# Kernel tuning notes

Hardware: AMD Instinct MI355X
Metric: run time of the kernel (lower is better)

## Reference

```python
import jax, jax.numpy as jnp
import numpy as np

N, F_IN, HID, HEADS, NEA, E, G = 50000, 32, 64, 2, 2, 800000, 50
SLOPE = 0.2  # leaky_relu negative_slope


def setup_inputs() -> dict:
    key = jax.random.key(0)
    ks = jax.random.split(key, 24)
    x = jax.random.normal(ks[0], (N, F_IN), jnp.float32)
    src = jax.random.randint(ks[1], (E,), 0, N, jnp.int32)
    off = jax.random.randint(ks[2], (E,), 1, N, jnp.int32)
    dst = ((src + off) % N).astype(jnp.int32)  # guaranteed no self loops
    edge_index = jnp.stack([src, dst])
    edge_attr = jax.random.uniform(ks[3], (E, NEA), jnp.float32, 0.5, 3.0)  # distances (reciprocal taken in fwd)
    batch = (jnp.arange(N) // (N // G)).astype(jnp.int32)
    interface_pos = jnp.arange(0, N, 5, dtype=jnp.int32)  # 200 interface nodes/graph

    def glorot(k, shape, fan_in, fan_out):
        s = jnp.sqrt(6.0 / (fan_in + fan_out))
        return jax.random.uniform(k, shape, jnp.float32, -s, s)

    HC = HEADS * HID
    W0 = glorot(ks[4], (F_IN, HC), F_IN, HC)
    attl0 = glorot(ks[5], (HEADS, HID), HID, HID)
    attr0 = glorot(ks[6], (HEADS, HID), HID, HID)
    W12 = glorot(ks[7], (2, HID, HC), HID, HC)
    attl12 = glorot(ks[8], (2, HEADS, HID), HID, HID)
    attr12 = glorot(ks[9], (2, HEADS, HID), HID, HID)
    eW = glorot(ks[10], (3, NEA, HC), NEA, HC)
    eb = jnp.zeros((3, HC), jnp.float32)
    bconv = jnp.zeros((3, HID), jnp.float32)
    gate_w = glorot(ks[11], (HID, 1), HID, 1)
    gate_b = jnp.zeros((1,), jnp.float32)
    lin1_w = glorot(ks[12], (4 * HID, 2 * HID), 4 * HID, 2 * HID)
    lin1_b = jnp.zeros((2 * HID,), jnp.float32)
    lin2_w = glorot(ks[13], (2 * HID, 1), 2 * HID, 1)
    lin2_b = jnp.zeros((1,), jnp.float32)
    return dict(x=x, edge_index=edge_index, edge_attr=edge_attr, batch=batch,
                interface_pos=interface_pos, graph_num=G,
                W0=W0, attl0=attl0, attr0=attr0, W12=W12, attl12=attl12, attr12=attr12,
                eW=eW, eb=eb, bconv=bconv, gate_w=gate_w, gate_b=gate_b,
                lin1_w=lin1_w, lin1_b=lin1_b, lin2_w=lin2_w, lin2_b=lin2_b)


def segment_softmax(e, seg, n):
    m = jax.ops.segment_max(e, seg, num_segments=n)
    ex = jnp.exp(e - m[seg])
    d = jax.ops.segment_sum(ex, seg, num_segments=n)
    return ex / (d[seg] + 1e-16)


def gate_conv(h, W, att_l, att_r, eW, eb, b, src, dst, ea):
    # GATEConv, concat=False, dropout in eval mode (identity)
    n = h.shape[0]
    H, C = att_l.shape
    xl = (h @ W).reshape(n, H, C)                      # lin_l == lin_r
    al = (xl * att_l).sum(-1)                          # [N,H]
    ar = (xl * att_r).sum(-1)
    e = jax.nn.leaky_relu(al[src] + ar[dst], SLOPE)    # [E+N,H]
    alpha = segment_softmax(e, dst, n)
    ee = (ea @ eW + eb).reshape(-1, H, C)              # edge embeddings
    msg = (xl[src] + ee) * alpha[..., None]
    out = jax.ops.segment_sum(msg, dst, num_segments=n)
    return out.mean(1) + b                             # mean over heads + bias


def reference(x, edge_index, edge_attr, batch, interface_pos, graph_num,
              W0, attl0, attr0, W12, attl12, attr12, eW, eb, bconv,
              gate_w, gate_b, lin1_w, lin1_b, lin2_w, lin2_b):
    n = x.shape[0]
    ar_n = jnp.arange(n, dtype=edge_index.dtype)
    src = jnp.concatenate([edge_index[0], ar_n])       # add self loops
    dst = jnp.concatenate([edge_index[1], ar_n])
    ea = jnp.concatenate([1.0 / edge_attr,
                          jnp.zeros((n, edge_attr.shape[1]), edge_attr.dtype)], 0)

    h = jnp.tanh(gate_conv(x, W0, attl0, attr0, eW[0], eb[0], bconv[0], src, dst, ea))
    xmax = h
    for l in range(2):  # num_layers - 1 structurally distinct weight slices
        h = jnp.tanh(gate_conv(h, W12[l], attl12[l], attr12[l],
                               eW[l + 1], eb[l + 1], bconv[l + 1], src, dst, ea))
        xmax = jnp.maximum(xmax, h)                    # JumpingKnowledge('max')

    xi = xmax[interface_pos]                           # [Ni, hidden]
    bi = batch[interface_pos]
    add = jax.ops.segment_sum(xi, bi, num_segments=graph_num)
    cnt = jax.ops.segment_sum(jnp.ones((xi.shape[0],), xi.dtype), bi, num_segments=graph_num)
    mean = add / jnp.maximum(cnt, 1.0)[:, None]
    gate = (xi @ gate_w + gate_b)[:, 0]                # global self-attention gate
    a = segment_softmax(gate, bi, graph_num)
    attp = jax.ops.segment_sum(a[:, None] * xi, bi, num_segments=graph_num)
    mx = jax.ops.segment_max(xi, bi, num_segments=graph_num)
    pooled = jnp.concatenate([add, mean, attp, mx], -1)  # [G, 4*hidden]
    z = jnp.tanh(pooled @ lin1_w + lin1_b)             # dropout eval = identity
    return z @ lin2_w + lin2_b                         # [G, 1]
```

## Files before the change

### kernel.cpp

```cpp
#include <hip/hip_runtime.h>
#include <hip/hip_bf16.h>
#include <hip/hip_fp16.h>
#include <math.h>

#define N_NODES 50000
#define FIN     32
#define HID     64
#define HC      128
#define NE      800000
#define NET     850000
#define NI      10000
#define NG      50
#define NPG     1000
#define NIPG    200
#define DMAX    64

#define LBLK    (N_NODES / 16)
#define ABLK    (N_NODES / 8)

typedef _Float16 half8 __attribute__((ext_vector_type(8)));
typedef float float4v __attribute__((ext_vector_type(4)));

__device__ __forceinline__ float lrelu(float x) { return fmaxf(x, 0.2f * x); }

__device__ __forceinline__ float rlf(float v, int l) {
  return __int_as_float(__builtin_amdgcn_readlane(__float_as_int(v), l));
}
__device__ __forceinline__ int rli(int v, int l) {
  return __builtin_amdgcn_readlane(v, l);
}

__global__ void k_build(const int* __restrict__ ei, const float* __restrict__ eattr,
                        int* __restrict__ deg, int2* __restrict__ erec) {
  int e = blockIdx.x * blockDim.x + threadIdx.x;
  if (e >= NET) return;
  int s, d; float ex, ey;
  if (e < NE) {
    s = ei[e]; d = ei[NE + e];
    float2 ea = ((const float2*)eattr)[e];
    ex = 1.0f / ea.x; ey = 1.0f / ea.y;
  } else {
    s = d = e - NE; ex = 0.f; ey = 0.f;
  }
  int r = atomicAdd(&deg[d], 1);
  if (r < DMAX) {
    __half2 ea2 = __floats2half2_rn(ex, ey);
    erec[d * DMAX + r] = make_int2(s << 8, *(int*)&ea2);
  }
}

template <int F>
__global__ __launch_bounds__(256) void k_linear_mfma(
    const float* __restrict__ h, const float* __restrict__ W,
    const float* __restrict__ attl, const float* __restrict__ attr,
    __half2* __restrict__ xl2h, float* __restrict__ al, float* __restrict__ ar) {
  __shared__ _Float16 hA[16 * F];
  __shared__ _Float16 hC[16 * 128];
  __shared__ float redl[16 * 4], redr[16 * 4];
  const int w = threadIdx.x >> 6, lane = threadIdx.x & 63;
  const int m = lane & 15, q = lane >> 4;
  const int n0 = blockIdx.x * 16;

  for (int i = threadIdx.x; i < 16 * F; i += 256)
    hA[i] = (_Float16)h[(size_t)n0 * F + i];
  __syncthreads();

  half8 a0, a1;
#pragma unroll
  for (int j = 0; j < 8; j++) a0[j] = hA[m * F + q * 8 + j];
  if constexpr (F == 64) {
#pragma unroll
    for (int j = 0; j < 8; j++) a1[j] = hA[m * F + 32 + q * 8 + j];
  }

  const int c0 = w * 32;
  float4v acc[2];
  float pl[4] = {0.f, 0.f, 0.f, 0.f}, pr[4] = {0.f, 0.f, 0.f, 0.f};
#pragma unroll
  for (int t = 0; t < 2; t++) {
    const int colg = c0 + t * 16 + m;
    half8 b0;
#pragma unroll
    for (int j = 0; j < 8; j++) b0[j] = (_Float16)W[(q * 8 + j) * HC + colg];
    float4v z = {0.f, 0.f, 0.f, 0.f};
    acc[t] = __builtin_amdgcn_mfma_f32_16x16x32_f16(a0, b0, z, 0, 0, 0);
    if constexpr (F == 64) {
      half8 b1;
#pragma unroll
      for (int j = 0; j < 8; j++) b1[j] = (_Float16)W[(32 + q * 8 + j) * HC + colg];
      acc[t] = __builtin_amdgcn_mfma_f32_16x16x32_f16(a1, b1, acc[t], 0, 0, 0);
    }
    const float atl = attl[colg], atr = attr[colg];
#pragma unroll
    for (int reg = 0; reg < 4; reg++) {
      float val = acc[t][reg];
      hC[(q * 4 + reg) * 128 + colg] = (_Float16)val;
      pl[reg] += val * atl;
      pr[reg] += val * atr;
    }
  }
#pragma unroll
  for (int off = 1; off < 16; off <<= 1) {
#pragma unroll
    for (int reg = 0; reg < 4; reg++) {
      pl[reg] += __shfl_xor(pl[reg], off, 64);
      pr[reg] += __shfl_xor(pr[reg], off, 64);
    }
  }
  if (m == 0) {
#pragma unroll
    for (int reg = 0; reg < 4; reg++) {
      redl[(q * 4 + reg) * 4 + w] = pl[reg];
      redr[(q * 4 + reg) * 4 + w] = pr[reg];
    }
  }
  __syncthreads();
  if (threadIdx.x < 32) {
    int node = threadIdx.x >> 1, head = threadIdx.x & 1;
    al[(n0 + node) * 2 + head] = redl[node * 4 + head * 2] + redl[node * 4 + head * 2 + 1];
    ar[(n0 + node) * 2 + head] = redr[node * 4 + head * 2] + redr[node * 4 + head * 2 + 1];
  }
  for (int i = threadIdx.x; i < 16 * 64; i += 256) {
    int node = i >> 6, cc = i & 63;
    xl2h[(size_t)(n0 + node) * HID + cc] =
        __halves2half2(hC[node * 128 + cc], hC[node * 128 + 64 + cc]);
  }
}

__device__ __forceinline__ void agg_wave(
    int n0, const __half2* __restrict__ xl, const float* __restrict__ alp,
    const float2* __restrict__ ar2,
    const int* __restrict__ degarr, const int2* __restrict__ erec,
    const float* __restrict__ eW2, const float* __restrict__ eb1,
    const float* __restrict__ bconv1, float& outA, float& outB) {
  const int gid0 = n0 + ((threadIdx.x >> 6) << 1);
  const int lane = threadIdx.x & 63;
  const int l32 = lane & 31;
  const int half = lane >> 5;
  const int lane4 = lane << 2;
  const int gidH = gid0 + half;
  const int o0H = gidH * DMAX;
  const int degH = min(degarr[gidH], DMAX);
  const float2 arvH = ar2[gidH];
  const char* xbase = (const char*)xl;
  const char* albase = (const char*)alp;

  const int degA = rli(degH, 0);
  const int degB = rli(degH, 32);
  const int degmax = max(degA, degB);

  float aA0 = 0.f, aA1 = 0.f, bA0 = 0.f, bA1 = 0.f;
  float aB0 = 0.f, aB1 = 0.f, bB0 = 0.f, bB1 = 0.f;
  float ld0 = 0.f, ld1 = 0.f, lex0 = 0.f, ley0 = 0.f, lex1 = 0.f, ley1 = 0.f;

  for (int base = 0; base < degmax; base += 32) {
    int j = base + l32;
    int soff = 0; float p0 = 0.f, p1 = 0.f;
    if (j < degH) {
      int2 r = erec[o0H + j];
      soff = r.x;
      float2 eaf = __half22float2(*(__half2*)&r.y);
      float2 alv = *(const float2*)(albase + (soff >> 5));
      p0 = __expf(lrelu(alv.x + arvH.x));
      p1 = __expf(lrelu(alv.y + arvH.y));
      ld0 += p0; ld1 += p1;
      lex0 += p0 * eaf.x; ley0 += p0 * eaf.y;
      lex1 += p1 * eaf.x; ley1 += p1 * eaf.y;
    }
    int lenA = min(32, degA - base); lenA = max(lenA, 0);
    int lenB = min(32, degB - base); lenB = max(lenB, 0);
    int lenA4 = (lenA + 3) & ~3;
    int lenB4 = (lenB + 3) & ~3;
    int len = max(lenA4, lenB4);
    for (int j2 = 0; j2 < len; j2 += 4) {
      if (j2 < lenA4) {
        float2 x0 = __half22float2(*(const __half2*)(xbase + rli(soff, j2)     + lane4));
        float2 x1 = __half22float2(*(const __half2*)(xbase + rli(soff, j2 + 1) + lane4));
        float2 x2 = __half22float2(*(const __half2*)(xbase + rli(soff, j2 + 2) + lane4));
        float2 x3 = __half22float2(*(const __half2*)(xbase + rli(soff, j2 + 3) + lane4));
        aA0 += rlf(p0, j2)     * x0.x; aA1 += rlf(p1, j2)     * x0.y;
        bA0 += rlf(p0, j2 + 1) * x1.x; bA1 += rlf(p1, j2 + 1) * x1.y;
        aA0 += rlf(p0, j2 + 2) * x2.x; aA1 += rlf(p1, j2 + 2) * x2.y;
        bA0 += rlf(p0, j2 + 3) * x3.x; bA1 += rlf(p1, j2 + 3) * x3.y;
      }
      if (j2 < lenB4) {
        float2 x4 = __half22float2(*(const __half2*)(xbase + rli(soff, 32 + j2)     + lane4));
        float2 x5 = __half22float2(*(const __half2*)(xbase + rli(soff, 32 + j2 + 1) + lane4));
        float2 x6 = __half22float2(*(const __half2*)(xbase + rli(soff, 32 + j2 + 2) + lane4));
        float2 x7 = __half22float2(*(const __half2*)(xbase + rli(soff, 32 + j2 + 3) + lane4));
        aB0 += rlf(p0, 32 + j2)     * x4.x; aB1 += rlf(p1, 32 + j2)     * x4.y;
        bB0 += rlf(p0, 32 + j2 + 1) * x5.x; bB1 += rlf(p1, 32 + j2 + 1) * x5.y;
        aB0 += rlf(p0, 32 + j2 + 2) * x6.x; aB1 += rlf(p1, 32 + j2 + 2) * x6.y;
        bB0 += rlf(p0, 32 + j2 + 3) * x7.x; bB1 += rlf(p1, 32 + j2 + 3) * x7.y;
      }
    }
  }
  float accA0 = aA0 + bA0, accA1 = aA1 + bA1;
  float accB0 = aB0 + bB0, accB1 = aB1 + bB1;
#pragma unroll
  for (int off = 16; off; off >>= 1) {
    ld0  += __shfl_xor(ld0, off, 64);
    ld1  += __shfl_xor(ld1, off, 64);
    lex0 += __shfl_xor(lex0, off, 64);
    ley0 += __shfl_xor(ley0, off, 64);
    lex1 += __shfl_xor(lex1, off, 64);
    ley1 += __shfl_xor(ley1, off, 64);
  }
  float ld0A  = __shfl(ld0,  l32, 64), ld0B  = __shfl(ld0,  32 + l32, 64);
  float ld1A  = __shfl(ld1,  l32, 64), ld1B  = __shfl(ld1,  32 + l32, 64);
  float lex0A = __shfl(lex0, l32, 64), lex0B = __shfl(lex0, 32 + l32, 64);
  float ley0A = __shfl(ley0, l32, 64), ley0B = __shfl(ley0, 32 + l32, 64);
  float lex1A = __shfl(lex1, l32, 64), lex1B = __shfl(lex1, 32 + l32, 64);
  float ley1A = __shfl(ley1, l32, 64), ley1B = __shfl(ley1, 32 + l32, 64);

  const float w00 = eW2[lane],      w01 = eW2[HC + lane],      b0v = eb1[lane];
  const float w10 = eW2[64 + lane], w11 = eW2[HC + 64 + lane], b1v = eb1[64 + lane];
  const float bc = bconv1[lane];

  float tA0 = accA0 + w00 * lex0A + w01 * ley0A + b0v * ld0A;
  float tA1 = accA1 + w10 * lex1A + w11 * ley1A + b1v * ld1A;
  float tB0 = accB0 + w00 * lex0B + w01 * ley0B + b0v * ld0B;
  float tB1 = accB1 + w10 * lex1B + w11 * ley1B + b1v * ld1B;
  outA = tanhf(0.5f * (tA0 / (ld0A + 1e-16f) + tA1 / (ld1A + 1e-16f)) + bc);
  outB = tanhf(0.5f * (tB0 / (ld0B + 1e-16f) + tB1 / (ld1B + 1e-16f)) + bc);
}

__global__ __launch_bounds__(256) void k_aggregate(
    const __half2* __restrict__ xl_in, const float* __restrict__ al_in,
    const float2* __restrict__ ar2, const int* __restrict__ degarr,
    const int2* __restrict__ erec, const float* __restrict__ eW2,
    const float* __restrict__ eb1, const float* __restrict__ bconv1,
    float* __restrict__ hout) {
  const int n0 = blockIdx.x * 8;
  float rA, rB;
  agg_wave(n0, xl_in, al_in, ar2, degarr, erec, eW2, eb1, bconv1, rA, rB);
  const int gid0 = n0 + ((threadIdx.x >> 6) << 1);
  const int lane = threadIdx.x & 63;
  hout[(size_t)gid0 * HID + lane] = rA;
  hout[(size_t)(gid0 + 1) * HID + lane] = rB;
}

__global__ __launch_bounds__(256) void k_agg_xi(
    const __half2* __restrict__ xl_in, const float* __restrict__ al_in,
    const float2* __restrict__ ar2, const int* __restrict__ degarr,
    const int2* __restrict__ erec, const float* __restrict__ eW2,
    const float* __restrict__ eb1, const float* __restrict__ bconv1,
    const float* __restrict__ h0, const float* __restrict__ h1,
    const float* __restrict__ gate_w, const float* __restrict__ gate_b,
    float* __restrict__ xi, float* __restrict__ gexp) {
  const int n0 = blockIdx.x * 8;
  float rA, rB;
  agg_wave(n0, xl_in, al_in, ar2, degarr, erec, eW2, eb1, bconv1, rA, rB);
  const int gid0 = n0 + ((threadIdx.x >> 6) << 1);
  const int lane = threadIdx.x & 63;
  const int nA = gid0, nB = gid0 + 1;
  const float gwv = gate_w[lane];
  const float gbv = gate_b[0];
  if (nA % 5 == 0) {
    float v = fmaxf(fmaxf(h0[(size_t)nA * HID + lane], h1[(size_t)nA * HID + lane]), rA);
    int idx = nA / 5;
    xi[(size_t)idx * HID + lane] = v;
    float gv = v * gwv;
#pragma unroll
    for (int off = 32; off; off >>= 1) gv += __shfl_xor(gv, off, 64);
    if (lane == 0) gexp[idx] = __expf(gv + gbv);
  }
  if (nB % 5 == 0) {
    float v = fmaxf(fmaxf(h0[(size_t)nB * HID + lane], h1[(size_t)nB * HID + lane]), rB);
    int idx = nB / 5;
    xi[(size_t)idx * HID + lane] = v;
    float gv = v * gwv;
#pragma unroll
    for (int off = 32; off; off >>= 1) gv += __shfl_xor(gv, off, 64);
    if (lane == 0) gexp[idx] = __expf(gv + gbv);
  }
}

__global__ __launch_bounds__(256) void k_final(
    const float* __restrict__ xi, const float* __restrict__ gexp,
    const float* __restrict__ lin1_w, const float* __restrict__ lin1_b,
    const float* __restrict__ lin2_w, const float* __restrict__ lin2_b,
    float* __restrict__ out) {
  __shared__ float red[4][3 * HID + 1];
  __shared__ float pooled[4 * HID];
  __shared__ float zred[2 * HID];
  const int g = blockIdx.x, t = threadIdx.x;
  const int w = t >> 6, lane = t & 63;

  float padd = 0.f, pmax = -1e30f, pattp = 0.f, paden = 0.f;
  for (int i = w; i < NIPG; i += 4) {
    int idx = g * NIPG + i;
    float v = xi[(size_t)idx * HID + lane];
    float e = gexp[idx];
    padd += v;
    pmax = fmaxf(pmax, v);
    pattp += e * v;
    paden += e;
  }
  red[w][lane] = padd;
  red[w][HID + lane] = pmax;
  red[w][2 * HID + lane] = pattp;
  if (lane == 0) red[w][3 * HID] = paden;
  __syncthreads();
  if (t < HID) {
    float a  = red[0][t] + red[1][t] + red[2][t] + red[3][t];
    float mx = fmaxf(fmaxf(red[0][HID + t], red[1][HID + t]),
                     fmaxf(red[2][HID + t], red[3][HID + t]));
    float ap = red[0][2 * HID + t] + red[1][2 * HID + t] +
               red[2][2 * HID + t] + red[3][2 * HID + t];
    float ad = red[0][3 * HID] + red[1][3 * HID] + red[2][3 * HID] + red[3][3 * HID];
    pooled[t]           = a;
    pooled[HID + t]     = a * (1.0f / NIPG);
    pooled[2 * HID + t] = ap / (ad + 1e-16f);
    pooled[3 * HID + t] = mx;
  }
  __syncthreads();
  if (t < 2 * HID) {
    float z = lin1_b[t];
    for (int k = 0; k < 4 * HID; k++) z += pooled[k] * lin1_w[k * (2 * HID) + t];
    z = tanhf(z);
    zred[t] = z * lin2_w[t];
  }
  __syncthreads();
  if (t == 0) {
    float s = 0.f;
    for (int k = 0; k < 2 * HID; k++) s += zred[k];
    out[g] = s + lin2_b[0];
  }
}

extern "C" void kernel_launch(void* const* d_in, const int* in_sizes, int n_in,
                              void* d_out, int out_size, void* d_ws, size_t ws_size,
                              hipStream_t stream) {
  const float* x      = (const float*)d_in[0];
  const int*   ei     = (const int*)d_in[1];
  const float* eattr  = (const float*)d_in[2];
  const float* W0     = (const float*)d_in[6];
  const float* attl0  = (const float*)d_in[7];
  const float* attr0  = (const float*)d_in[8];
  const float* W12    = (const float*)d_in[9];
  const float* attl12 = (const float*)d_in[10];
  const float* attr12 = (const float*)d_in[11];
  const float* eW     = (const float*)d_in[12];
  const float* eb     = (const float*)d_in[13];
  const float* bconv  = (const float*)d_in[14];
  const float* gate_w = (const float*)d_in[15];
  const float* gate_b = (const float*)d_in[16];
  const float* lin1_w = (const float*)d_in[17];
  const float* lin1_b = (const float*)d_in[18];
  const float* lin2_w = (const float*)d_in[19];
  const float* lin2_b = (const float*)d_in[20];
  float* out = (float*)d_out;

  char* ws = (char*)d_ws;
  size_t off = 0;
  auto alloc = [&](size_t elems) {
    void* p = ws + off;
    off += ((elems * 4 + 15) / 16) * 16;
    return p;
  };
  int*      deg    = (int*)alloc(N_NODES);
  size_t zbytes = off;
  int2*    erec   = (int2*)alloc((size_t)N_NODES * DMAX * 2);
  __half2* xl2hA  = (__half2*)alloc((size_t)N_NODES * HID);
  __half2* xl2hB  = (__half2*)alloc((size_t)N_NODES * HID);
  float*   alA    = (float*)alloc((size_t)N_NODES * 2);
  float*   alB    = (float*)alloc((size_t)N_NODES * 2);
  float*   arr    = (float*)alloc((size_t)N_NODES * 2);
  float*   h0     = (float*)alloc((size_t)N_NODES * HID);
  float*   h1     = (float*)alloc((size_t)N_NODES * HID);
  float*   xi     = (float*)alloc((size_t)NI * HID);
  float*   gexp   = (float*)alloc(NI);
  (void)ws_size; (void)in_sizes; (void)n_in; (void)out_size;

  hipMemsetAsync(d_ws, 0, zbytes, stream);

  k_build<<<(NET + 255) / 256, 256, 0, stream>>>(ei, eattr, deg, erec);
  k_linear_mfma<FIN><<<LBLK, 256, 0, stream>>>(x, W0, attl0, attr0, xl2hA, alA, arr);
  k_aggregate<<<ABLK, 256, 0, stream>>>(xl2hA, alA, (const float2*)arr, deg, erec,
                                        eW, eb, bconv, h0);
  k_linear_mfma<HID><<<LBLK, 256, 0, stream>>>(h0, W12, attl12, attr12, xl2hB, alB, arr);
  k_aggregate<<<ABLK, 256, 0, stream>>>(xl2hB, alB, (const float2*)arr, deg, erec,
                                        eW + 2 * HC, eb + HC, bconv + HID, h1);
  k_linear_mfma<HID><<<LBLK, 256, 0, stream>>>(h1, W12 + (size_t)HID * HC,
                                               attl12 + HC, attr12 + HC, xl2hA, alA, arr);
  k_agg_xi<<<ABLK, 256, 0, stream>>>(xl2hA, alA, (const float2*)arr, deg, erec,
                                     eW + 4 * HC, eb + 2 * HC, bconv + 2 * HID,
                                     h0, h1, gate_w, gate_b, xi, gexp);
  k_final<<<NG, 256, 0, stream>>>(xi, gexp, lin1_w, lin1_b, lin2_w, lin2_b, out);
}
```

Baseline: 330.1 us.

## Fuse edge-build and first linear layer into one launch, vectorize edge loads

Merges the CSR-style edge bucketing kernel and the layer-0 MFMA linear kernel into a single launch: the first blocks process edges and the remaining blocks compute linear tiles, since the two are independent. The edge path now handles four edges per thread with int4/float4 loads and a scalar fallback for the tail and self-loops. This removes one kernel launch and boundary and lets the two stages overlap on the device. In exchange the fused kernel carries the shared-memory footprint of the linear tile for every block, and each thread issues four atomics in sequence.

```diff
diff --git a/kernel.cpp b/kernel.cpp
--- a/kernel.cpp
+++ b/kernel.cpp
@@ -15,6 +15,7 @@
 #define NIPG    200
 #define DMAX    64
 
+#define EBLK4   ((NET + 1023) / 1024)
 #define LBLK    (N_NODES / 16)
 #define ABLK    (N_NODES / 8)
 
@@ -30,23 +31,135 @@
   return __builtin_amdgcn_readlane(v, l);
 }
 
-__global__ void k_build(const int* __restrict__ ei, const float* __restrict__ eattr,
-                        int* __restrict__ deg, int2* __restrict__ erec) {
-  int e = blockIdx.x * blockDim.x + threadIdx.x;
-  if (e >= NET) return;
-  int s, d; float ex, ey;
-  if (e < NE) {
-    s = ei[e]; d = ei[NE + e];
-    float2 ea = ((const float2*)eattr)[e];
-    ex = 1.0f / ea.x; ey = 1.0f / ea.y;
-  } else {
-    s = d = e - NE; ex = 0.f; ey = 0.f;
-  }
-  int r = atomicAdd(&deg[d], 1);
-  if (r < DMAX) {
-    __half2 ea2 = __floats2half2_rn(ex, ey);
-    erec[d * DMAX + r] = make_int2(s << 8, *(int*)&ea2);
-  }
+template <int F>
+__device__ __forceinline__ void lin_tile(
+    int n0, const float* __restrict__ h, const float* __restrict__ W,
+    const float* __restrict__ attl, const float* __restrict__ attr,
+    __half2* __restrict__ xl2h, float* __restrict__ al, float* __restrict__ ar,
+    _Float16* hA, _Float16* hC, float* redl, float* redr) {
+  const int w = threadIdx.x >> 6, lane = threadIdx.x & 63;
+  const int m = lane & 15, q = lane >> 4;
+
+  for (int i = threadIdx.x; i < 16 * F; i += 256)
+    hA[i] = (_Float16)h[(size_t)n0 * F + i];
+  __syncthreads();
+
+  half8 a0, a1;
+#pragma unroll
+  for (int j = 0; j < 8; j++) a0[j] = hA[m * F + q * 8 + j];
+  if constexpr (F == 64) {
+#pragma unroll
+    for (int j = 0; j < 8; j++) a1[j] = hA[m * F + 32 + q * 8 + j];
+  }
+
+  const int c0 = w * 32;
+  float4v acc[2];
+  float pl[4] = {0.f, 0.f, 0.f, 0.f}, pr[4] = {0.f, 0.f, 0.f, 0.f};
+#pragma unroll
+  for (int t = 0; t < 2; t++) {
+    const int colg = c0 + t * 16 + m;
+    half8 b0;
+#pragma unroll
+    for (int j = 0; j < 8; j++) b0[j] = (_Float16)W[(q * 8 + j) * HC + colg];
+    float4v z = {0.f, 0.f, 0.f, 0.f};
+    acc[t] = __builtin_amdgcn_mfma_f32_16x16x32_f16(a0, b0, z, 0, 0, 0);
+    if constexpr (F == 64) {
+      half8 b1;
+#pragma unroll
+      for (int j = 0; j < 8; j++) b1[j] = (_Float16)W[(32 + q * 8 + j) * HC + colg];
+      acc[t] = __builtin_amdgcn_mfma_f32_16x16x32_f16(a1, b1, acc[t], 0, 0, 0);
+    }
+    const float atl = attl[colg], atr = attr[colg];
+#pragma unroll
+    for (int reg = 0; reg < 4; reg++) {
+      float val = acc[t][reg];
+      hC[(q * 4 + reg) * 128 + colg] = (_Float16)val;
+      pl[reg] += val * atl;
+      pr[reg] += val * atr;
+    }
+  }
+#pragma unroll
+  for (int off = 1; off < 16; off <<= 1) {
+#pragma unroll
+    for (int reg = 0; reg < 4; reg++) {
+      pl[reg] += __shfl_xor(pl[reg], off, 64);
+      pr[reg] += __shfl_xor(pr[reg], off, 64);
+    }
+  }
+  if (m == 0) {
+#pragma unroll
+    for (int reg = 0; reg < 4; reg++) {
+      redl[(q * 4 + reg) * 4 + w] = pl[reg];
+      redr[(q * 4 + reg) * 4 + w] = pr[reg];
+    }
+  }
+  __syncthreads();
+  if (threadIdx.x < 32) {
+    int node = threadIdx.x >> 1, head = threadIdx.x & 1;
+    al[(n0 + node) * 2 + head] = redl[node * 4 + head * 2] + redl[node * 4 + head * 2 + 1];
+    ar[(n0 + node) * 2 + head] = redr[node * 4 + head * 2] + redr[node * 4 + head * 2 + 1];
+  }
+  for (int i = threadIdx.x; i < 16 * 64; i += 256) {
+    int node = i >> 6, cc = i & 63;
+    xl2h[(size_t)(n0 + node) * HID + cc] =
+        __halves2half2(hC[node * 128 + cc], hC[node * 128 + 64 + cc]);
+  }
+}
+
+__global__ __launch_bounds__(256) void k_build_lin0(
+    const int* __restrict__ ei, const float* __restrict__ eattr,
+    int* __restrict__ deg, int2* __restrict__ erec,
+    const float* __restrict__ x, const float* __restrict__ W0,
+    const float* __restrict__ attl0, const float* __restrict__ attr0,
+    __half2* __restrict__ xl2h, float* __restrict__ al, float* __restrict__ ar) {
+  __shared__ _Float16 hA[16 * FIN];
+  __shared__ _Float16 hC[16 * 128];
+  __shared__ float redl[16 * 4], redr[16 * 4];
+  const int b = blockIdx.x;
+  if (b < EBLK4) {
+    const int e0 = (b * 256 + threadIdx.x) * 4;
+    if (e0 + 3 < NE) {
+      int4 s4 = *(const int4*)(ei + e0);
+      int4 d4 = *(const int4*)(ei + NE + e0);
+      float4 ea01 = *(const float4*)(eattr + 2 * e0);
+      float4 ea23 = *(const float4*)(eattr + 2 * e0 + 4);
+      int r0 = atomicAdd(&deg[d4.x], 1);
+      int r1 = atomicAdd(&deg[d4.y], 1);
+      int r2 = atomicAdd(&deg[d4.z], 1);
+      int r3 = atomicAdd(&deg[d4.w], 1);
+      __half2 p0 = __floats2half2_rn(1.0f / ea01.x, 1.0f / ea01.y);
+      __half2 p1 = __floats2half2_rn(1.0f / ea01.z, 1.0f / ea01.w);
+      __half2 p2 = __floats2half2_rn(1.0f / ea23.x, 1.0f / ea23.y);
+      __half2 p3 = __floats2half2_rn(1.0f / ea23.z, 1.0f / ea23.w);
+      if (r0 < DMAX) erec[d4.x * DMAX + r0] = make_int2(s4.x << 8, *(int*)&p0);
+      if (r1 < DMAX) erec[d4.y * DMAX + r1] = make_int2(s4.y << 8, *(int*)&p1);
+      if (r2 < DMAX) erec[d4.z * DMAX + r2] = make_int2(s4.z << 8, *(int*)&p2);
+      if (r3 < DMAX) erec[d4.w * DMAX + r3] = make_int2(s4.w << 8, *(int*)&p3);
+    } else {
+#pragma unroll
+      for (int k = 0; k < 4; k++) {
+        int e = e0 + k;
+        if (e < NET) {
+          int s, d; float ex, ey;
+          if (e < NE) {
+            s = ei[e]; d = ei[NE + e];
+            float2 ea = ((const float2*)eattr)[e];
+            ex = 1.0f / ea.x; ey = 1.0f / ea.y;
+          } else {
+            s = d = e - NE; ex = 0.f; ey = 0.f;
+          }
+          int r = atomicAdd(&deg[d], 1);
+          if (r < DMAX) {
+            __half2 ea2 = __floats2half2_rn(ex, ey);
+            erec[d * DMAX + r] = make_int2(s << 8, *(int*)&ea2);
+          }
+        }
+      }
+    }
+    return;
+  }
+  lin_tile<FIN>((b - EBLK4) * 16, x, W0, attl0, attr0, xl2h, al, ar,
+                hA, hC, redl, redr);
 }
 
 template <int F>
@@ -57,74 +170,7 @@
   __shared__ _Float16 hA[16 * F];
   __shared__ _Float16 hC[16 * 128];
   __shared__ float redl[16 * 4], redr[16 * 4];
-  const int w = threadIdx.x >> 6, lane = threadIdx.x & 63;
-  const int m = lane & 15, q = lane >> 4;
-  const int n0 = blockIdx.x * 16;
-
-  for (int i = threadIdx.x; i < 16 * F; i += 256)
-    hA[i] = (_Float16)h[(size_t)n0 * F + i];
-  __syncthreads();
-
-  half8 a0, a1;
-#pragma unroll
-  for (int j = 0; j < 8; j++) a0[j] = hA[m * F + q * 8 + j];
-  if constexpr (F == 64) {
-#pragma unroll
-    for (int j = 0; j < 8; j++) a1[j] = hA[m * F + 32 + q * 8 + j];
-  }
-
-  const int c0 = w * 32;
-  float4v acc[2];
-  float pl[4] = {0.f, 0.f, 0.f, 0.f}, pr[4] = {0.f, 0.f, 0.f, 0.f};
-#pragma unroll
-  for (int t = 0; t < 2; t++) {
-    const int colg = c0 + t * 16 + m;
-    half8 b0;
-#pragma unroll
-    for (int j = 0; j < 8; j++) b0[j] = (_Float16)W[(q * 8 + j) * HC + colg];
-    float4v z = {0.f, 0.f, 0.f, 0.f};
-    acc[t] = __builtin_amdgcn_mfma_f32_16x16x32_f16(a0, b0, z, 0, 0, 0);
-    if constexpr (F == 64) {
-      half8 b1;
-#pragma unroll
-      for (int j = 0; j < 8; j++) b1[j] = (_Float16)W[(32 + q * 8 + j) * HC + colg];
-      acc[t] = __builtin_amdgcn_mfma_f32_16x16x32_f16(a1, b1, acc[t], 0, 0, 0);
-    }
-    const float atl = attl[colg], atr = attr[colg];
-#pragma unroll
-    for (int reg = 0; reg < 4; reg++) {
-      float val = acc[t][reg];
-      hC[(q * 4 + reg) * 128 + colg] = (_Float16)val;
-      pl[reg] += val * atl;
-      pr[reg] += val * atr;
-    }
-  }
-#pragma unroll
-  for (int off = 1; off < 16; off <<= 1) {
-#pragma unroll
-    for (int reg = 0; reg < 4; reg++) {
-      pl[reg] += __shfl_xor(pl[reg], off, 64);
-      pr[reg] += __shfl_xor(pr[reg], off, 64);
-    }
-  }
-  if (m == 0) {
-#pragma unroll
-    for (int reg = 0; reg < 4; reg++) {
-      redl[(q * 4 + reg) * 4 + w] = pl[reg];
-      redr[(q * 4 + reg) * 4 + w] = pr[reg];
-    }
-  }
-  __syncthreads();
-  if (threadIdx.x < 32) {
-    int node = threadIdx.x >> 1, head = threadIdx.x & 1;
-    al[(n0 + node) * 2 + head] = redl[node * 4 + head * 2] + redl[node * 4 + head * 2 + 1];
-    ar[(n0 + node) * 2 + head] = redr[node * 4 + head * 2] + redr[node * 4 + head * 2 + 1];
-  }
-  for (int i = threadIdx.x; i < 16 * 64; i += 256) {
-    int node = i >> 6, cc = i & 63;
-    xl2h[(size_t)(n0 + node) * HID + cc] =
-        __halves2half2(hC[node * 128 + cc], hC[node * 128 + 64 + cc]);
-  }
+  lin_tile<F>(blockIdx.x * 16, h, W, attl, attr, xl2h, al, ar, hA, hC, redl, redr);
 }
 
 __device__ __forceinline__ void agg_wave(
@@ -375,8 +421,8 @@
 
   hipMemsetAsync(d_ws, 0, zbytes, stream);
 
-  k_build<<<(NET + 255) / 256, 256, 0, stream>>>(ei, eattr, deg, erec);
-  k_linear_mfma<FIN><<<LBLK, 256, 0, stream>>>(x, W0, attl0, attr0, xl2hA, alA, arr);
+  k_build_lin0<<<EBLK4 + LBLK, 256, 0, stream>>>(ei, eattr, deg, erec,
+                                                 x, W0, attl0, attr0, xl2hA, alA, arr);
   k_aggregate<<<ABLK, 256, 0, stream>>>(xl2hA, alA, (const float2*)arr, deg, erec,
                                         eW, eb, bconv, h0);
   k_linear_mfma<HID><<<LBLK, 256, 0, stream>>>(h0, W12, attl12, attr12, xl2hB, alB, arr);
```

New measurement: 337.3 us. 1.02x slower.

## Fuse next-layer MFMA linear projection into aggregation kernel epilogue

Applied to the files above, without the earlier changes.

Each aggregation block now stages its 8 output node rows in shared memory as fp16. It then runs the next layer's 64→128 projection with MFMA 16x16x32 instructions, padding the tile to 16 rows. The same epilogue computes the left and right attention logits and writes the fp16 xl buffer directly. This removes two separate linear-kernel launches and the global re-read of h0/h1. In exchange, every block reloads and converts the weight matrix from global memory, and half of each MFMA tile is wasted on padding rows.

```diff
diff --git a/kernel.cpp b/kernel.cpp
--- a/kernel.cpp
+++ b/kernel.cpp
@@ -225,19 +225,88 @@
   outB = tanhf(0.5f * (tB0 / (ld0B + 1e-16f) + tB1 / (ld1B + 1e-16f)) + bc);
 }
 
-__global__ __launch_bounds__(256) void k_aggregate(
+__global__ __launch_bounds__(256) void k_agg_lin(
     const __half2* __restrict__ xl_in, const float* __restrict__ al_in,
     const float2* __restrict__ ar2, const int* __restrict__ degarr,
     const int2* __restrict__ erec, const float* __restrict__ eW2,
     const float* __restrict__ eb1, const float* __restrict__ bconv1,
-    float* __restrict__ hout) {
+    float* __restrict__ hout,
+    const float* __restrict__ Wn, const float* __restrict__ attln,
+    const float* __restrict__ attrn, __half2* __restrict__ xl_out,
+    float* __restrict__ al_out, float* __restrict__ ar_out) {
+  __shared__ _Float16 hA[16 * HID];
+  __shared__ _Float16 hC[8 * 128];
+  __shared__ float redl[16 * 4], redr[16 * 4];
   const int n0 = blockIdx.x * 8;
+  const int w = threadIdx.x >> 6, lane = threadIdx.x & 63;
+
   float rA, rB;
   agg_wave(n0, xl_in, al_in, ar2, degarr, erec, eW2, eb1, bconv1, rA, rB);
-  const int gid0 = n0 + ((threadIdx.x >> 6) << 1);
-  const int lane = threadIdx.x & 63;
+  const int gid0 = n0 + 2 * w;
   hout[(size_t)gid0 * HID + lane] = rA;
   hout[(size_t)(gid0 + 1) * HID + lane] = rB;
+  hA[(2 * w) * HID + lane] = (_Float16)rA;
+  hA[(2 * w + 1) * HID + lane] = (_Float16)rB;
+  hA[(8 + 2 * w) * HID + lane] = (_Float16)0.f;
+  hA[(9 + 2 * w) * HID + lane] = (_Float16)0.f;
+  __syncthreads();
+
+  const int m = lane & 15, q = lane >> 4;
+  half8 a0, a1;
+#pragma unroll
+  for (int j = 0; j < 8; j++) a0[j] = hA[m * HID + q * 8 + j];
+#pragma unroll
+  for (int j = 0; j < 8; j++) a1[j] = hA[m * HID + 32 + q * 8 + j];
+
+  const int c0 = w * 32;
+  float pl[4] = {0.f, 0.f, 0.f, 0.f}, pr[4] = {0.f, 0.f, 0.f, 0.f};
+#pragma unroll
+  for (int t = 0; t < 2; t++) {
+    const int colg = c0 + t * 16 + m;
+    half8 b0, b1;
+#pragma unroll
+    for (int j = 0; j < 8; j++) b0[j] = (_Float16)Wn[(q * 8 + j) * HC + colg];
+#pragma unroll
+    for (int j = 0; j < 8; j++) b1[j] = (_Float16)Wn[(32 + q * 8 + j) * HC + colg];
+    float4v z = {0.f, 0.f, 0.f, 0.f};
+    float4v acc = __builtin_amdgcn_mfma_f32_16x16x32_f16(a0, b0, z, 0, 0, 0);
+    acc = __builtin_amdgcn_mfma_f32_16x16x32_f16(a1, b1, acc, 0, 0, 0);
+    const float atl = attln[colg], atr = attrn[colg];
+#pragma unroll
+    for (int reg = 0; reg < 4; reg++) {
+      float val = acc[reg];
+      int row = q * 4 + reg;
+      if (row < 8) hC[row * 128 + colg] = (_Float16)val;
+      pl[reg] += val * atl;
+      pr[reg] += val * atr;
+    }
+  }
+#pragma unroll
+  for (int off = 1; off < 16; off <<= 1) {
+#pragma unroll
+    for (int reg = 0; reg < 4; reg++) {
+      pl[reg] += __shfl_xor(pl[reg], off, 64);
+      pr[reg] += __shfl_xor(pr[reg], off, 64);
+    }
+  }
+  if (m == 0) {
+#pragma unroll
+    for (int reg = 0; reg < 4; reg++) {
+      redl[(q * 4 + reg) * 4 + w] = pl[reg];
+      redr[(q * 4 + reg) * 4 + w] = pr[reg];
+    }
+  }
+  __syncthreads();
+  if (threadIdx.x < 16) {
+    int node = threadIdx.x >> 1, head = threadIdx.x & 1;
+    al_out[(n0 + node) * 2 + head] = redl[node * 4 + head * 2] + redl[node * 4 + head * 2 + 1];
+    ar_out[(n0 + node) * 2 + head] = redr[node * 4 + head * 2] + redr[node * 4 + head * 2 + 1];
+  }
+  for (int i = threadIdx.x; i < 8 * 64; i += 256) {
+    int node = i >> 6, cc = i & 63;
+    xl_out[(size_t)(n0 + node) * HID + cc] =
+        __halves2half2(hC[node * 128 + cc], hC[node * 128 + 64 + cc]);
+  }
 }
 
 __global__ __launch_bounds__(256) void k_agg_xi(
@@ -377,13 +446,13 @@
 
   k_build<<<(NET + 255) / 256, 256, 0, stream>>>(ei, eattr, deg, erec);
   k_linear_mfma<FIN><<<LBLK, 256, 0, stream>>>(x, W0, attl0, attr0, xl2hA, alA, arr);
-  k_aggregate<<<ABLK, 256, 0, stream>>>(xl2hA, alA, (const float2*)arr, deg, erec,
-                                        eW, eb, bconv, h0);
-  k_linear_mfma<HID><<<LBLK, 256, 0, stream>>>(h0, W12, attl12, attr12, xl2hB, alB, arr);
-  k_aggregate<<<ABLK, 256, 0, stream>>>(xl2hB, alB, (const float2*)arr, deg, erec,
-                                        eW + 2 * HC, eb + HC, bconv + HID, h1);
-  k_linear_mfma<HID><<<LBLK, 256, 0, stream>>>(h1, W12 + (size_t)HID * HC,
-                                               attl12 + HC, attr12 + HC, xl2hA, alA, arr);
+  k_agg_lin<<<ABLK, 256, 0, stream>>>(xl2hA, alA, (const float2*)arr, deg, erec,
+                                      eW, eb, bconv, h0,
+                                      W12, attl12, attr12, xl2hB, alB, arr);
+  k_agg_lin<<<ABLK, 256, 0, stream>>>(xl2hB, alB, (const float2*)arr, deg, erec,
+                                      eW + 2 * HC, eb + HC, bconv + HID, h1,
+                                      W12 + (size_t)HID * HC, attl12 + HC, attr12 + HC,
+                                      xl2hA, alA, arr);
   k_agg_xi<<<ABLK, 256, 0, stream>>>(xl2hA, alA, (const float2*)arr, deg, erec,
                                      eW + 4 * HC, eb + 2 * HC, bconv + 2 * HID,
                                      h0, h1, gate_w, gate_b, xi, gexp);
```

Measured after the change: 334.3 us. About the same (+1.3%).
